# Optimization experiments

Measured on AMD Instinct MI355X. Metric: run time of the kernel, lower is better.

The kernel has to match this reference:

```python
import jax, jax.numpy as jnp
import numpy as np

B, E, N, F = 8, 2048, 2048, 128

def setup_inputs() -> dict:
    key = jax.random.key(0)
    k1, k2, k3, k4 = jax.random.split(key, 4)
    node_embeddings = jax.random.normal(k1, (B, N, F), dtype=jnp.float32)
    adj = jax.random.randint(k2, (B, E, N), -1, 3).astype(jnp.float32)
    W = jax.random.normal(k3, (F, F), dtype=jnp.float32) * (1.0 / np.sqrt(F))
    b = jax.random.normal(k4, (F,), dtype=jnp.float32) * 0.01
    return {"node_embeddings": node_embeddings, "adj": adj, "W": W, "b": b}

def reference(node_embeddings, adj, W, b):
    # adj_target: 1 where adj == -1, else 0
    adj_target = (adj == -1).astype(node_embeddings.dtype)          # [B, E, N]
    norm = jnp.sum(adj_target, axis=-1, keepdims=True)               # [B, E, 1]
    norm = jnp.where(norm == 0, 1.0, norm)
    # masked-mean aggregation of neighbor vertices into hyperedges
    message_vertex = jnp.matmul(adj_target, node_embeddings) / norm  # [B, E, F]
    # linear (torch Linear: x @ W.T + b) + relu
    hyperedge_embeddings = jax.nn.relu(jnp.matmul(message_vertex, W.T) + b)
    return hyperedge_embeddings
```

## Files before the change

kernel.cpp:

```cpp
#include <hip/hip_runtime.h>
#include <hip/hip_bf16.h>

#define B_ 8
#define E_ 2048
#define N_ 2048
#define F_ 128

#define BM 64
#define MT 4
#define BK 64
#define MP 136

using bf16x8 = __bf16 __attribute__((ext_vector_type(8)));
using fx4    = float __attribute__((ext_vector_type(4)));

__global__ __launch_bounds__(256) void prep_all(const float* __restrict__ node,
                                                const float* __restrict__ adj,
                                                const float* __restrict__ W,
                                                __bf16* __restrict__ nodeT,
                                                __bf16* __restrict__ Wb,
                                                unsigned char* __restrict__ bitsT,
                                                float* __restrict__ rcount) {
    __shared__ __align__(16) unsigned char rowB[256];
    __shared__ float cw[4];
    const int bid = blockIdx.x;
    const int t   = threadIdx.x;

    if (bid < 512) {
        const int b  = bid & 7;
        const int n0 = (bid >> 3) * 32;
        const int f  = t & 127;
        const int nb = n0 + (t >> 7) * 16;
        const float* src = node + ((size_t)b * N_ + nb) * F_ + f;
        __bf16 h[16];
#pragma unroll
        for (int i = 0; i < 16; ++i)
            h[i] = (__bf16)src[(size_t)i * F_];
        __bf16* dst = nodeT + ((size_t)b * F_ + f) * N_ + nb;
        *(uint4*)&dst[0] = *(const uint4*)&h[0];
        *(uint4*)&dst[8] = *(const uint4*)&h[8];
    } else if (bid < 528) {
        int idx = (bid - 512) * 256 + t;
        float4 v = *(const float4*)&W[idx * 4];
        __bf16 o[4] = {(__bf16)v.x, (__bf16)v.y, (__bf16)v.z, (__bf16)v.w};
        *(uint2*)&Wb[idx * 4] = *(const uint2*)o;
    } else {
        const int row = bid - 528;
        const float* src = adj + (size_t)row * N_ + t * 8;
        float4 v0 = *(const float4*)src;
        float4 v1 = *(const float4*)(src + 4);
        unsigned m = 0;
        m |= (v0.x == -1.f) ? 1u   : 0u;
        m |= (v0.y == -1.f) ? 2u   : 0u;
        m |= (v0.z == -1.f) ? 4u   : 0u;
        m |= (v0.w == -1.f) ? 8u   : 0u;
        m |= (v1.x == -1.f) ? 16u  : 0u;
        m |= (v1.y == -1.f) ? 32u  : 0u;
        m |= (v1.z == -1.f) ? 64u  : 0u;
        m |= (v1.w == -1.f) ? 128u : 0u;

        const int q  = t & 3;
        const int ks = (t >> 2) & 1;
        const int mm = t >> 3;
        rowB[q * 64 + mm * 2 + ks] = (unsigned char)m;

        float c = (float)__popc(m);
#pragma unroll
        for (int s = 1; s < 64; s <<= 1) c += __shfl_xor(c, s);
        if ((t & 63) == 0) cw[t >> 6] = c;
        __syncthreads();

        if (t < 64) {
            unsigned d = *(const unsigned*)&rowB[t * 4];
            *(unsigned*)&bitsT[(size_t)row * 256 + t * 4] = d;
        }
        if (t == 0) {
            float tot = cw[0] + cw[1] + cw[2] + cw[3];
            rcount[row] = 1.f / fmaxf(tot, 1.f);
        }
    }
}

__global__ __launch_bounds__(256, 1) void v2h_main(const unsigned char* __restrict__ bitsT,
                                                   const __bf16* __restrict__ nodeT,
                                                   const __bf16* __restrict__ Wb,
                                                   const float* __restrict__ bias,
                                                   const float* __restrict__ rcount,
                                                   float* __restrict__ out) {
    __shared__ __align__(16) __bf16 smem[2 * 128 * 64];
    __bf16 (*Bs)[128][64] = (__bf16 (*)[128][64])smem;
    __bf16* Ms = smem;

    const int t    = threadIdx.x;
    const int bid  = blockIdx.x;
    const int b    = bid & 7;
    const int e0   = (bid >> 3) * BM;
    const int w    = t >> 6;
    const int lane = t & 63;
    const int l15  = lane & 15;
    const int quad = lane >> 4;

    const __bf16* nTB = nodeT + (size_t)b * F_ * N_;

    auto issue_dma = [&](int k0, int buf) {
#pragma unroll
        for (int p = 0; p < 4; ++p) {
            int idx = t + 256 * p;
            int f   = idx >> 3;
            int sl  = idx & 7;
            int g   = sl ^ (f & 7);
            const __bf16* src = nTB + (size_t)f * N_ + k0 + g * 8;
            __bf16* dst = &Bs[buf][0][0] + (size_t)(w * 64 + 256 * p) * 8;
            __builtin_amdgcn_global_load_lds(
                (const __attribute__((address_space(1))) void*)src,
                (__attribute__((address_space(3))) void*)dst, 16, 0, 0);
        }
    };

    unsigned rw[MT][16];
#pragma unroll
    for (int mt = 0; mt < MT; ++mt) {
        const unsigned char* rp = bitsT + ((size_t)b * E_ + e0 + mt * 16 + l15) * 256 + quad * 64;
        uint4 r0 = *(const uint4*)(rp +  0), r1 = *(const uint4*)(rp + 16);
        uint4 r2 = *(const uint4*)(rp + 32), r3 = *(const uint4*)(rp + 48);
        rw[mt][0] = r0.x; rw[mt][1] = r0.y; rw[mt][2]  = r0.z; rw[mt][3]  = r0.w;
        rw[mt][4] = r1.x; rw[mt][5] = r1.y; rw[mt][6]  = r1.z; rw[mt][7]  = r1.w;
        rw[mt][8] = r2.x; rw[mt][9] = r2.y; rw[mt][10] = r2.z; rw[mt][11] = r2.w;
        rw[mt][12] = r3.x; rw[mt][13] = r3.y; rw[mt][14] = r3.z; rw[mt][15] = r3.w;
    }

    auto unpack = [](unsigned byte) -> bf16x8 {
        union { unsigned u[4]; bf16x8 v; } r;
        r.u[0] = ((byte &   1u) ? 0x3F80u : 0u) | ((byte &   2u) ? 0x3F800000u : 0u);
        r.u[1] = ((byte &   4u) ? 0x3F80u : 0u) | ((byte &   8u) ? 0x3F800000u : 0u);
        r.u[2] = ((byte &  16u) ? 0x3F80u : 0u) | ((byte &  32u) ? 0x3F800000u : 0u);
        r.u[3] = ((byte &  64u) ? 0x3F80u : 0u) | ((byte & 128u) ? 0x3F800000u : 0u);
        return r.v;
    };

    fx4 acc[MT][2] = {};

    issue_dma(0, 0);

#pragma unroll
    for (int m = 0; m < 32; ++m) {
        const int buf = m & 1;
        __syncthreads();

        if (m != 31)
            issue_dma((m + 1) * BK, buf ^ 1);

        const int sh = 16 * (m & 1);
        bf16x8 af0[MT], af1[MT];
#pragma unroll
        for (int mt = 0; mt < MT; ++mt) {
            const unsigned wd = rw[mt][m >> 1] >> sh;
            af0[mt] = unpack(wd & 255u);
            af1[mt] = unpack((wd >> 8) & 255u);
        }

#pragma unroll
        for (int ft = 0; ft < 2; ++ft) {
            int f  = w * 32 + ft * 16 + l15;
            int q0 = quad ^ (f & 7);
            int q1 = (4 + quad) ^ (f & 7);
            bf16x8 b0 = *(const bf16x8*)&Bs[buf][f][q0 * 8];
#pragma unroll
            for (int mt = 0; mt < MT; ++mt)
                acc[mt][ft] = __builtin_amdgcn_mfma_f32_16x16x32_bf16(af0[mt], b0, acc[mt][ft], 0, 0, 0);
            bf16x8 b1 = *(const bf16x8*)&Bs[buf][f][q1 * 8];
#pragma unroll
            for (int mt = 0; mt < MT; ++mt)
                acc[mt][ft] = __builtin_amdgcn_mfma_f32_16x16x32_bf16(af1[mt], b1, acc[mt][ft], 0, 0, 0);
        }
    }

    const int rbase = quad * 4;
    const float* rcB = rcount + (size_t)b * E_ + e0;
    float4 rn[MT];
#pragma unroll
    for (int mt = 0; mt < MT; ++mt)
        rn[mt] = *(const float4*)&rcB[mt * 16 + rbase];

#pragma unroll
    for (int ft = 0; ft < 2; ++ft) {
        int fcol = w * 32 + ft * 16 + l15;
#pragma unroll
        for (int mt = 0; mt < MT; ++mt) {
            const float* rr = (const float*)&rn[mt];
#pragma unroll
            for (int r = 0; r < 4; ++r)
                Ms[(mt * 16 + rbase + r) * MP + fcol] = (__bf16)(acc[mt][ft][r] * rr[r]);
        }
    }
    __syncthreads();

    fx4 acc2[MT][2] = {};
#pragma unroll
    for (int ks = 0; ks < 4; ++ks) {
        bf16x8 afm[MT];
#pragma unroll
        for (int mt = 0; mt < MT; ++mt)
            afm[mt] = *(const bf16x8*)&Ms[(mt * 16 + l15) * MP + ks * 32 + quad * 8];
#pragma unroll
        for (int gt = 0; gt < 2; ++gt) {
            int g = w * 32 + gt * 16 + l15;
            bf16x8 wfr = *(const bf16x8*)&Wb[(size_t)g * F_ + ks * 32 + quad * 8];
#pragma unroll
            for (int mt = 0; mt < MT; ++mt)
                acc2[mt][gt] = __builtin_amdgcn_mfma_f32_16x16x32_bf16(afm[mt], wfr, acc2[mt][gt], 0, 0, 0);
        }
    }

#pragma unroll
    for (int gt = 0; gt < 2; ++gt) {
        int g = w * 32 + gt * 16 + l15;
        float bb = bias[g];
#pragma unroll
        for (int mt = 0; mt < MT; ++mt) {
#pragma unroll
            for (int r = 0; r < 4; ++r) {
                int e = e0 + mt * 16 + rbase + r;
                float v = acc2[mt][gt][r] + bb;
                out[((size_t)b * E_ + e) * F_ + g] = fmaxf(v, 0.f);
            }
        }
    }
}

extern "C" void kernel_launch(void* const* d_in, const int* in_sizes, int n_in,
                              void* d_out, int out_size, void* d_ws, size_t ws_size,
                              hipStream_t stream) {
    const float* node = (const float*)d_in[0];
    const float* adj  = (const float*)d_in[1];
    const float* W    = (const float*)d_in[2];
    const float* bias = (const float*)d_in[3];
    float* out = (float*)d_out;

    char* ws = (char*)d_ws;
    __bf16*        nodeT = (__bf16*)ws;
    __bf16*        Wb    = (__bf16*)(ws + 8 * 1024 * 1024);
    unsigned char* bitsT = (unsigned char*)(ws + 8 * 1024 * 1024 + 65536);
    float*         rcnt  = (float*)(ws + 12 * 1024 * 1024 + 65536);

    prep_all<<<528 + B_ * E_, 256, 0, stream>>>(node, adj, W, nodeT, Wb, bitsT, rcnt);
    v2h_main<<<256, 256, 0, stream>>>(bitsT, nodeT, Wb, bias, rcnt, out);
}
```

Before: 218.8 us.

## Fuse adjacency bit-packing and row counts into the main GEMM kernel

Drops the separate pass that turns adj into packed bitmasks and reciprocal counts. The main kernel now loads the fp32 adj tiles itself with register prefetch two steps ahead, converts them to bits in shared memory, and counts row popcounts on the fly. This removes a full write and re-read of the bitmask and count arrays and shrinks the prep launch. In exchange, the 128 MB adj read now happens inside only 256 blocks at one block per CU, which may limit bandwidth and stall the MFMA loop.

```diff
diff --git a/kernel.cpp b/kernel.cpp
--- a/kernel.cpp
+++ b/kernel.cpp
@@ -15,14 +15,9 @@
 using fx4    = float __attribute__((ext_vector_type(4)));
 
 __global__ __launch_bounds__(256) void prep_all(const float* __restrict__ node,
-                                                const float* __restrict__ adj,
                                                 const float* __restrict__ W,
                                                 __bf16* __restrict__ nodeT,
-                                                __bf16* __restrict__ Wb,
-                                                unsigned char* __restrict__ bitsT,
-                                                float* __restrict__ rcount) {
-    __shared__ __align__(16) unsigned char rowB[256];
-    __shared__ float cw[4];
+                                                __bf16* __restrict__ Wb) {
     const int bid = blockIdx.x;
     const int t   = threadIdx.x;
 
@@ -39,57 +34,23 @@
         __bf16* dst = nodeT + ((size_t)b * F_ + f) * N_ + nb;
         *(uint4*)&dst[0] = *(const uint4*)&h[0];
         *(uint4*)&dst[8] = *(const uint4*)&h[8];
-    } else if (bid < 528) {
+    } else {
         int idx = (bid - 512) * 256 + t;
         float4 v = *(const float4*)&W[idx * 4];
         __bf16 o[4] = {(__bf16)v.x, (__bf16)v.y, (__bf16)v.z, (__bf16)v.w};
         *(uint2*)&Wb[idx * 4] = *(const uint2*)o;
-    } else {
-        const int row = bid - 528;
-        const float* src = adj + (size_t)row * N_ + t * 8;
-        float4 v0 = *(const float4*)src;
-        float4 v1 = *(const float4*)(src + 4);
-        unsigned m = 0;
-        m |= (v0.x == -1.f) ? 1u   : 0u;
-        m |= (v0.y == -1.f) ? 2u   : 0u;
-        m |= (v0.z == -1.f) ? 4u   : 0u;
-        m |= (v0.w == -1.f) ? 8u   : 0u;
-        m |= (v1.x == -1.f) ? 16u  : 0u;
-        m |= (v1.y == -1.f) ? 32u  : 0u;
-        m |= (v1.z == -1.f) ? 64u  : 0u;
-        m |= (v1.w == -1.f) ? 128u : 0u;
-
-        const int q  = t & 3;
-        const int ks = (t >> 2) & 1;
-        const int mm = t >> 3;
-        rowB[q * 64 + mm * 2 + ks] = (unsigned char)m;
-
-        float c = (float)__popc(m);
-#pragma unroll
-        for (int s = 1; s < 64; s <<= 1) c += __shfl_xor(c, s);
-        if ((t & 63) == 0) cw[t >> 6] = c;
-        __syncthreads();
-
-        if (t < 64) {
-            unsigned d = *(const unsigned*)&rowB[t * 4];
-            *(unsigned*)&bitsT[(size_t)row * 256 + t * 4] = d;
-        }
-        if (t == 0) {
-            float tot = cw[0] + cw[1] + cw[2] + cw[3];
-            rcount[row] = 1.f / fmaxf(tot, 1.f);
-        }
     }
 }
 
-__global__ __launch_bounds__(256, 1) void v2h_main(const unsigned char* __restrict__ bitsT,
+__global__ __launch_bounds__(256, 1) void v2h_main(const float* __restrict__ adj,
                                                    const __bf16* __restrict__ nodeT,
                                                    const __bf16* __restrict__ Wb,
                                                    const float* __restrict__ bias,
-                                                   const float* __restrict__ rcount,
                                                    float* __restrict__ out) {
-    __shared__ __align__(16) __bf16 smem[2 * 128 * 64];
-    __bf16 (*Bs)[128][64] = (__bf16 (*)[128][64])smem;
-    __bf16* Ms = smem;
+    __shared__ __align__(16) __bf16 Bs[2][128][64];
+    __shared__ __align__(16) unsigned long long Abits[2][64];
+    __shared__ __align__(16) float normS[BM];
+    __shared__ __align__(16) __bf16 Ms[BM * MP];
 
     const int t    = threadIdx.x;
     const int bid  = blockIdx.x;
@@ -99,6 +60,11 @@
     const int lane = t & 63;
     const int l15  = lane & 15;
     const int quad = lane >> 4;
+
+    const int ar   = lane >> 2;
+    const int acs  = lane & 3;
+    const int arow = w * 16 + ar;
+    const float* aPtr = adj + ((size_t)b * E_ + e0 + arow) * N_ + acs * 16;
 
     const __bf16* nTB = nodeT + (size_t)b * F_ * N_;
 
@@ -117,17 +83,26 @@
         }
     };
 
-    unsigned rw[MT][16];
-#pragma unroll
-    for (int mt = 0; mt < MT; ++mt) {
-        const unsigned char* rp = bitsT + ((size_t)b * E_ + e0 + mt * 16 + l15) * 256 + quad * 64;
-        uint4 r0 = *(const uint4*)(rp +  0), r1 = *(const uint4*)(rp + 16);
-        uint4 r2 = *(const uint4*)(rp + 32), r3 = *(const uint4*)(rp + 48);
-        rw[mt][0] = r0.x; rw[mt][1] = r0.y; rw[mt][2]  = r0.z; rw[mt][3]  = r0.w;
-        rw[mt][4] = r1.x; rw[mt][5] = r1.y; rw[mt][6]  = r1.z; rw[mt][7]  = r1.w;
-        rw[mt][8] = r2.x; rw[mt][9] = r2.y; rw[mt][10] = r2.z; rw[mt][11] = r2.w;
-        rw[mt][12] = r3.x; rw[mt][13] = r3.y; rw[mt][14] = r3.z; rw[mt][15] = r3.w;
-    }
+    auto cvt16 = [](float4 v0, float4 v1, float4 v2, float4 v3) -> unsigned {
+        unsigned m = 0;
+        m |= (v0.x == -1.f) ? 1u     : 0u;
+        m |= (v0.y == -1.f) ? 2u     : 0u;
+        m |= (v0.z == -1.f) ? 4u     : 0u;
+        m |= (v0.w == -1.f) ? 8u     : 0u;
+        m |= (v1.x == -1.f) ? 16u    : 0u;
+        m |= (v1.y == -1.f) ? 32u    : 0u;
+        m |= (v1.z == -1.f) ? 64u    : 0u;
+        m |= (v1.w == -1.f) ? 128u   : 0u;
+        m |= (v2.x == -1.f) ? 256u   : 0u;
+        m |= (v2.y == -1.f) ? 512u   : 0u;
+        m |= (v2.z == -1.f) ? 1024u  : 0u;
+        m |= (v2.w == -1.f) ? 2048u  : 0u;
+        m |= (v3.x == -1.f) ? 4096u  : 0u;
+        m |= (v3.y == -1.f) ? 8192u  : 0u;
+        m |= (v3.z == -1.f) ? 16384u : 0u;
+        m |= (v3.w == -1.f) ? 32768u : 0u;
+        return m;
+    };
 
     auto unpack = [](unsigned byte) -> bf16x8 {
         union { unsigned u[4]; bf16x8 v; } r;
@@ -139,24 +114,50 @@
     };
 
     fx4 acc[MT][2] = {};
-
+    int cnt = 0;
+
+    float4 a0 = *(const float4*)(aPtr + 0);
+    float4 a1 = *(const float4*)(aPtr + 4);
+    float4 a2 = *(const float4*)(aPtr + 8);
+    float4 a3 = *(const float4*)(aPtr + 12);
     issue_dma(0, 0);
+    {
+        unsigned bits = cvt16(a0, a1, a2, a3);
+        ((unsigned short*)&Abits[0][arow])[acs] = (unsigned short)bits;
+        cnt += __popc(bits);
+    }
+    a0 = *(const float4*)(aPtr + BK + 0);
+    a1 = *(const float4*)(aPtr + BK + 4);
+    a2 = *(const float4*)(aPtr + BK + 8);
+    a3 = *(const float4*)(aPtr + BK + 12);
 
 #pragma unroll
     for (int m = 0; m < 32; ++m) {
         const int buf = m & 1;
         __syncthreads();
 
-        if (m != 31)
+        if (m < 31)
             issue_dma((m + 1) * BK, buf ^ 1);
-
-        const int sh = 16 * (m & 1);
+        if (m < 31) {
+            unsigned bits = cvt16(a0, a1, a2, a3);
+            ((unsigned short*)&Abits[buf ^ 1][arow])[acs] = (unsigned short)bits;
+            cnt += __popc(bits);
+        }
+        if (m < 30) {
+            const float* ap = aPtr + (m + 2) * BK;
+            a0 = *(const float4*)(ap + 0);
+            a1 = *(const float4*)(ap + 4);
+            a2 = *(const float4*)(ap + 8);
+            a3 = *(const float4*)(ap + 12);
+        }
+
         bf16x8 af0[MT], af1[MT];
 #pragma unroll
         for (int mt = 0; mt < MT; ++mt) {
-            const unsigned wd = rw[mt][m >> 1] >> sh;
-            af0[mt] = unpack(wd & 255u);
-            af1[mt] = unpack((wd >> 8) & 255u);
+            unsigned long long v = Abits[buf][mt * 16 + l15];
+            unsigned lo = (unsigned)v, hi = (unsigned)(v >> 32);
+            af0[mt] = unpack((lo >> (8 * quad)) & 255u);
+            af1[mt] = unpack((hi >> (8 * quad)) & 255u);
         }
 
 #pragma unroll
@@ -175,12 +176,20 @@
         }
     }
 
+    {
+        float c = (float)cnt;
+        c += __shfl_xor(c, 1);
+        c += __shfl_xor(c, 2);
+        if (acs == 0)
+            normS[arow] = 1.f / fmaxf(c, 1.f);
+    }
+    __syncthreads();
+
     const int rbase = quad * 4;
-    const float* rcB = rcount + (size_t)b * E_ + e0;
     float4 rn[MT];
 #pragma unroll
     for (int mt = 0; mt < MT; ++mt)
-        rn[mt] = *(const float4*)&rcB[mt * 16 + rbase];
+        rn[mt] = *(const float4*)&normS[mt * 16 + rbase];
 
 #pragma unroll
     for (int ft = 0; ft < 2; ++ft) {
@@ -238,11 +247,9 @@
     float* out = (float*)d_out;
 
     char* ws = (char*)d_ws;
-    __bf16*        nodeT = (__bf16*)ws;
-    __bf16*        Wb    = (__bf16*)(ws + 8 * 1024 * 1024);
-    unsigned char* bitsT = (unsigned char*)(ws + 8 * 1024 * 1024 + 65536);
-    float*         rcnt  = (float*)(ws + 12 * 1024 * 1024 + 65536);
-
-    prep_all<<<528 + B_ * E_, 256, 0, stream>>>(node, adj, W, nodeT, Wb, bitsT, rcnt);
-    v2h_main<<<256, 256, 0, stream>>>(bitsT, nodeT, Wb, bias, rcnt, out);
+    __bf16* nodeT = (__bf16*)ws;
+    __bf16* Wb    = (__bf16*)(ws + 8 * 1024 * 1024);
+
+    prep_all<<<528, 256, 0, stream>>>(node, W, nodeT, Wb);
+    v2h_main<<<256, 256, 0, stream>>>(adj, nodeT, Wb, bias, out);
 }
```

Result: faster. 210.6 us (-3.8%).
